# Optimization experiments

Measured on AMD Instinct MI355X. Metric: run time of the kernel, lower is better.

Reference implementation:

```python
import jax, jax.numpy as jnp
import numpy as np

B, W, NN, EPG = 8, 16, 64, 1024   # batch, window, nodes/graph, trace-edges/graph
N = B * W * NN                     # 8192 flattened nodes
E = B * W * EPG                    # 131072 node-graph edges == trace rows
E2 = 4 * E                         # 524288 edge-graph (line-graph) edges
D_NODE = 128; D_LOG = 128; D_EDGE = 128
D_IN = D_NODE + D_LOG              # 256 = GATv2 node2node in_channels
H = 4
EPS = 1e-16                        # PyG softmax epsilon


def _lin(key, fan_in, fan_out):
    return jax.random.normal(key, (fan_in, fan_out), jnp.float32) * (1.0 / np.sqrt(fan_in))


def setup_inputs() -> dict:
    key = jax.random.key(0)
    ks = jax.random.split(key, 16)
    return {
        "x_node": jax.random.normal(ks[0], (B, W, NN, D_NODE), jnp.float32),
        "x_trace": jax.random.normal(ks[1], (B, W, EPG, D_EDGE), jnp.float32),
        "x_log": jax.random.normal(ks[2], (B, W, NN, D_LOG), jnp.float32),
        "node_adj": jax.random.randint(ks[3], (2, E), 0, N, jnp.int32),
        "edge_adj": jax.random.randint(ks[4], (2, E2), 0, E, jnp.int32),
        "edge_efea": jax.random.randint(ks[5], (E2,), 0, N, jnp.int32),
        # node2node GATv2Conv: in=256, heads=4, out/head=64, edge_dim=128
        "n2n_Wl": _lin(ks[6], D_IN, D_IN), "n2n_bl": jnp.zeros((D_IN,), jnp.float32),
        "n2n_Wr": _lin(ks[7], D_IN, D_IN), "n2n_br": jnp.zeros((D_IN,), jnp.float32),
        "n2n_We": _lin(ks[8], D_EDGE, D_IN),
        "n2n_att": jax.random.normal(ks[9], (H, D_IN // H), jnp.float32) * 0.1,
        "n2n_bias": jnp.zeros((D_IN,), jnp.float32),
        # egde2node GATv2Conv: in=128, heads=4, out/head=32, edge_dim=256
        "e2n_Wl": _lin(ks[10], D_EDGE, D_EDGE), "e2n_bl": jnp.zeros((D_EDGE,), jnp.float32),
        "e2n_Wr": _lin(ks[11], D_EDGE, D_EDGE), "e2n_br": jnp.zeros((D_EDGE,), jnp.float32),
        "e2n_We": _lin(ks[12], D_IN, D_EDGE),
        "e2n_att": jax.random.normal(ks[13], (H, D_EDGE // H), jnp.float32) * 0.1,
        "e2n_bias": jnp.zeros((D_EDGE,), jnp.float32),
    }


def gatv2(x, edge_index, edge_attr, Wl, bl, Wr, br, We, att, bias, num_nodes):
    """PyG GATv2Conv (eval mode, add_self_loops=False, concat heads)."""
    heads, C = att.shape
    src, dst = edge_index[0], edge_index[1]
    xl = (x @ Wl + bl).reshape(-1, heads, C)   # source transform [N,H,C]
    xr = (x @ Wr + br).reshape(-1, heads, C)   # target transform [N,H,C]
    e = (edge_attr @ We).reshape(-1, heads, C) # edge transform   [E,H,C]
    m = jax.nn.leaky_relu(xl[src] + xr[dst] + e, 0.2)  # [E,H,C]
    alpha = jnp.einsum('ehc,hc->eh', m, att)           # [E,H]
    amax = jax.ops.segment_max(alpha, dst, num_segments=num_nodes)
    ex = jnp.exp(alpha - amax[dst])
    denom = jax.ops.segment_sum(ex, dst, num_segments=num_nodes)
    a = ex / (denom[dst] + EPS)                        # per-target softmax
    out = jax.ops.segment_sum(a[:, :, None] * xl[src], dst, num_segments=num_nodes)
    return out.reshape(num_nodes, heads * C) + bias


def reference(x_node, x_trace, x_log, node_adj, edge_adj, edge_efea,
              n2n_Wl, n2n_bl, n2n_Wr, n2n_br, n2n_We, n2n_att, n2n_bias,
              e2n_Wl, e2n_bl, e2n_Wr, e2n_br, e2n_We, e2n_att, e2n_bias):
    node = jnp.concatenate([x_node, x_log], axis=-1).reshape(-1, D_IN)  # [N,256]
    trace = x_trace.reshape(-1, D_EDGE)                                 # [E,128]
    node = gatv2(node, node_adj, trace,
                 n2n_Wl, n2n_bl, n2n_Wr, n2n_br, n2n_We, n2n_att, n2n_bias, N)
    trace = gatv2(trace, edge_adj, node[edge_efea],
                  e2n_Wl, e2n_bl, e2n_Wr, e2n_br, e2n_We, e2n_att, e2n_bias, E)
    xn = node[:, :D_NODE].reshape(B, W, NN, D_NODE)
    xt = trace.reshape(B, W, EPG, D_EDGE)
    xlg = node[:, D_NODE:].reshape(B, W, NN, D_LOG)
    return (xn, xt, xlg)
```

## Files before the change

### kernel.cpp

```cpp
#include <hip/hip_runtime.h>
#include <hip/hip_bf16.h>

constexpr int N    = 8192;
constexpr int E    = 131072;
constexpr int E2   = 524288;

constexpr size_t XT_OFF  = (size_t)N * 128;
constexpr size_t XLG_OFF = XT_OFF + (size_t)E * 128;

typedef unsigned short u16;
typedef short s16x8 __attribute__((ext_vector_type(8)));
typedef float f32x4 __attribute__((ext_vector_type(4)));

__device__ __forceinline__ u16 f2bs(float f) {
    unsigned x = __float_as_uint(f);
    return (u16)((x + 0x7FFF + ((x >> 16) & 1)) >> 16);
}
__device__ __forceinline__ float bs2f(u16 u) {
    return __uint_as_float((unsigned)u << 16);
}

__global__ __launch_bounds__(256) void k_prep(
    const float* __restrict__ Wl, const float* __restrict__ Wr,
    const float* __restrict__ We, const float* __restrict__ Wl2,
    const float* __restrict__ Wr2, const float* __restrict__ We2,
    u16* __restrict__ Wlt, u16* __restrict__ Wrt, u16* __restrict__ Wet,
    u16* __restrict__ Wl2t, u16* __restrict__ Wr2t, u16* __restrict__ We2t)
{
    const int gid = blockIdx.x * 256 + threadIdx.x;
    const float* src; u16* dst; int base, Kk, sh, perm;
    if      (gid <  65536) { src = Wl;  dst = Wlt;  base = 0;      Kk = 256; sh = 8; perm = 0; }
    else if (gid < 131072) { src = Wr;  dst = Wrt;  base = 65536;  Kk = 256; sh = 8; perm = 0; }
    else if (gid < 163840) { src = We;  dst = Wet;  base = 131072; Kk = 128; sh = 8; perm = 1; }
    else if (gid < 180224) { src = Wl2; dst = Wl2t; base = 163840; Kk = 128; sh = 7; perm = 1; }
    else if (gid < 196608) { src = Wr2; dst = Wr2t; base = 180224; Kk = 128; sh = 7; perm = 1; }
    else                   { src = We2; dst = We2t; base = 196608; Kk = 256; sh = 7; perm = 0; }
    const int l = gid - base;
    const int k = l >> sh, nn = l & ((1 << sh) - 1);
    int ns = nn;
    if (perm) ns = (nn & ~63) | ((nn & 3) << 4) | ((nn >> 2) & 15);
    dst[(size_t)ns * Kk + k] = f2bs(src[l]);
}

__global__ void k_hist2(const int* __restrict__ d1, const int* __restrict__ d2,
                        int* __restrict__ c1, int* __restrict__ c2)
{
    int i = blockIdx.x * 256 + threadIdx.x;
    if (i < E) atomicAdd(&c1[d1[i]], 1);
    else { int j = i - E; atomicAdd(&c2[d2[j]], 1); }
}

__global__ __launch_bounds__(1024) void k_scan_part(
    const int* __restrict__ cnt, int* __restrict__ off, int* __restrict__ tsums)
{
    __shared__ int tile[8192];
    __shared__ int wsum[16];
    const int tid = threadIdx.x, lane = tid & 63, wv = tid >> 6;
    const int base = blockIdx.x * 8192;
    for (int i = tid; i < 8192; i += 1024) tile[i] = cnt[base + i];
    __syncthreads();
    const int st = tid * 8;
    int s = 0;
    for (int k = 0; k < 8; ++k) { int v = tile[st + k]; tile[st + k] = s; s += v; }
    const int tsum = s;
    int incl = s;
    for (int o = 1; o < 64; o <<= 1) {
        int v = __shfl_up(incl, o);
        if (lane >= o) incl += v;
    }
    if (lane == 63) wsum[wv] = incl;
    __syncthreads();
    int woff = 0;
    for (int wq = 0; wq < wv; ++wq) woff += wsum[wq];
    const int add = woff + incl - tsum;
    for (int k = 0; k < 8; ++k) off[base + st + k] = add + tile[st + k];
    if (tid == 1023) tsums[blockIdx.x] = woff + incl;
}

__global__ __launch_bounds__(1024) void k_scan_add(
    int* __restrict__ off, int* __restrict__ cur,
    const int* __restrict__ tsums, int ntiles, int n)
{
    const int b = blockIdx.x;
    int carry = 0;
    for (int t = 0; t < b; ++t) carry += tsums[t];
    const int base = b * 8192 + threadIdx.x * 8;
#pragma unroll
    for (int k = 0; k < 8; ++k) {
        int v = off[base + k] + carry;
        off[base + k] = v;
        cur[base + k] = v;
    }
    if (b == ntiles - 1 && threadIdx.x == 1023)
        off[n] = carry + tsums[b];
}

__global__ void k_scatterM(
    const int* __restrict__ adj, int* __restrict__ cur1,
    int* __restrict__ srcc, int* __restrict__ pos1,
    const int* __restrict__ eadj, const int* __restrict__ efea,
    int* __restrict__ cur2, int2* __restrict__ sf2)
{
    int i = blockIdx.x * 256 + threadIdx.x;
    if (i < E) {
        int pos = atomicAdd(&cur1[adj[E + i]], 1);
        srcc[pos] = adj[i];
        pos1[i] = pos;
    } else {
        int j = i - E;
        int pos = atomicAdd(&cur2[eadj[E2 + j]], 1);
        sf2[pos] = make_int2(eadj[j], efea[j]);
    }
}

__global__ __launch_bounds__(256) void k_node_gemm(
    const float* __restrict__ x_node, const float* __restrict__ x_log,
    const u16* __restrict__ Wlt, const float* __restrict__ bl,
    const u16* __restrict__ Wrt, const float* __restrict__ br,
    u16* __restrict__ xl, u16* __restrict__ xr)
{
    __shared__ u16 A[32][260];
    const int n0 = blockIdx.x * 32;
    const int tid = threadIdx.x;
    for (int i = tid; i < 32 * 64; i += 256) {
        const int r = i >> 6, k4 = (i & 63) << 2;
        const float* srcp = (k4 < 128) ? &x_node[(size_t)(n0 + r) * 128 + k4]
                                       : &x_log [(size_t)(n0 + r) * 128 + (k4 - 128)];
        const float4 v = *(const float4*)srcp;
        ushort4 o; o.x = f2bs(v.x); o.y = f2bs(v.y); o.z = f2bs(v.z); o.w = f2bs(v.w);
        *(ushort4*)&A[r][k4] = o;
    }
    __syncthreads();
    const int w = tid >> 6, lane = tid & 63, lr = lane & 15, lq = lane >> 4;
    const u16* Wt     = (w < 2) ? Wlt : Wrt;
    const float* bias = (w < 2) ? bl : br;
    u16* outp         = (w < 2) ? xl : xr;
    const int cb = (w & 1) * 128;
    f32x4 acc[2][8] = {};
    for (int kb = 0; kb < 8; ++kb) {
        s16x8 afr0 = *(const s16x8*)&A[lr][kb * 32 + lq * 8];
        s16x8 afr1 = *(const s16x8*)&A[16 + lr][kb * 32 + lq * 8];
#pragma unroll
        for (int ct = 0; ct < 8; ++ct) {
            const int n = cb + ct * 16 + lr;
            s16x8 bfr = *(const s16x8*)&Wt[(size_t)n * 256 + kb * 32 + lq * 8];
            acc[0][ct] = __builtin_amdgcn_mfma_f32_16x16x32_bf16(afr0, bfr, acc[0][ct], 0, 0, 0);
            acc[1][ct] = __builtin_amdgcn_mfma_f32_16x16x32_bf16(afr1, bfr, acc[1][ct], 0, 0, 0);
        }
    }
#pragma unroll
    for (int rt = 0; rt < 2; ++rt)
#pragma unroll
        for (int ct = 0; ct < 8; ++ct) {
            const int col = cb + ct * 16 + lr;
            const float bv = bias[col];
#pragma unroll
            for (int reg = 0; reg < 4; ++reg) {
                const int row = n0 + rt * 16 + lq * 4 + reg;
                outp[(size_t)row * 256 + col] = f2bs(acc[rt][ct][reg] + bv);
            }
        }
}

constexpr int TPB_EDGE = 4;
__global__ __launch_bounds__(512) void k_edge_mm(
    const float* __restrict__ x_trace,
    const int* __restrict__ adj,
    const int* __restrict__ pos1,
    const u16* __restrict__ xl_n, const u16* __restrict__ xr_n,
    const u16* __restrict__ Wet,
    const u16* __restrict__ Wl2t, const float* __restrict__ bl2,
    const u16* __restrict__ Wr2t, const float* __restrict__ br2,
    const float* __restrict__ att,
    float* __restrict__ alpha, u16* __restrict__ xl_e, u16* __restrict__ xrst)
{
    __shared__ u16 A[2][32][132];
    __shared__ int ss[2][32], dd[2][32], pp[2][32];
    const int tid = threadIdx.x;
    const int w8 = tid >> 6;
    const int role = w8 >> 2;
    const int w = w8 & 3;
    const int lane = tid & 63, lr = lane & 15, lq = lane >> 4;

    s16x8 wf[4][4];
    const int cb2 = (w & 1) * 64;
    if (role == 0) {
#pragma unroll
        for (int kb = 0; kb < 4; ++kb)
#pragma unroll
            for (int ct = 0; ct < 4; ++ct)
                wf[kb][ct] = *(const s16x8*)&Wet[(size_t)(w * 64 + ct * 16 + lr) * 128 + kb * 32 + lq * 8];
    } else {
        const u16* Wt2 = (w < 2) ? Wl2t : Wr2t;
#pragma unroll
        for (int kb = 0; kb < 4; ++kb)
#pragma unroll
            for (int ct = 0; ct < 4; ++ct)
                wf[kb][ct] = *(const s16x8*)&Wt2[(size_t)(cb2 + ct * 16 + lr) * 128 + kb * 32 + lq * 8];
    }
    const float4 attq = *(const float4*)&att[w * 64 + lr * 4];
    const float4 b2q  = (role == 0) ? make_float4(0, 0, 0, 0)
        : *(const float4*)&((w < 2) ? bl2 : br2)[cb2 + lr * 4];

    const int tile0 = blockIdx.x * TPB_EDGE;
    {
        const int e0s = tile0 * 32;
        const int i0 = tid, i1 = tid + 512;
        {
            const int r = i0 >> 5, k4 = (i0 & 31) << 2;
            const float4 v = *(const float4*)&x_trace[(size_t)(e0s + r) * 128 + k4];
            ushort4 o; o.x = f2bs(v.x); o.y = f2bs(v.y); o.z = f2bs(v.z); o.w = f2bs(v.w);
            *(ushort4*)&A[0][r][k4] = o;
        }
        {
            const int r = i1 >> 5, k4 = (i1 & 31) << 2;
            const float4 v = *(const float4*)&x_trace[(size_t)(e0s + r) * 128 + k4];
            ushort4 o; o.x = f2bs(v.x); o.y = f2bs(v.y); o.z = f2bs(v.z); o.w = f2bs(v.w);
            *(ushort4*)&A[0][r][k4] = o;
        }
        if (tid < 32) {
            ss[0][tid] = adj[e0s + tid];
            dd[0][tid] = adj[E + e0s + tid];
            pp[0][tid] = pos1[e0s + tid];
        }
    }

    for (int t = 0; t < TPB_EDGE; ++t) {
        __syncthreads();
        const int b = t & 1;
        const int e0 = (tile0 + t) * 32;
        if (t + 1 < TPB_EDGE) {
            const int e0s = (tile0 + t + 1) * 32;
            const int bn = b ^ 1;
            {
                const int r = tid >> 5, k4 = (tid & 31) << 2;
                const float4 v = *(const float4*)&x_trace[(size_t)(e0s + r) * 128 + k4];
                ushort4 o; o.x = f2bs(v.x); o.y = f2bs(v.y); o.z = f2bs(v.z); o.w = f2bs(v.w);
                *(ushort4*)&A[bn][r][k4] = o;
            }
            {
                const int i1 = tid + 512;
                const int r = i1 >> 5, k4 = (i1 & 31) << 2;
                const float4 v = *(const float4*)&x_trace[(size_t)(e0s + r) * 128 + k4];
                ushort4 o; o.x = f2bs(v.x); o.y = f2bs(v.y); o.z = f2bs(v.z); o.w = f2bs(v.w);
                *(ushort4*)&A[bn][r][k4] = o;
            }
            if (tid < 32) {
                ss[bn][tid] = adj[e0s + tid];
                dd[bn][tid] = adj[E + e0s + tid];
                pp[bn][tid] = pos1[e0s + tid];
            }
        }

        if (role == 0) {
            const int co = w * 64 + lr * 4;
            ushort4 xlv[2][4], xrv[2][4];
#pragma unroll
            for (int rt = 0; rt < 2; ++rt)
#pragma unroll
                for (int reg = 0; reg < 4; ++reg) {
                    const int rowt = rt * 16 + lq * 4 + reg;
                    xlv[rt][reg] = *(const ushort4*)&xl_n[(size_t)ss[b][rowt] * 256 + co];
                    xrv[rt][reg] = *(const ushort4*)&xr_n[(size_t)dd[b][rowt] * 256 + co];
                }
            f32x4 acc1[2][4] = {};
#pragma unroll
            for (int kb = 0; kb < 4; ++kb) {
                s16x8 afr0 = *(const s16x8*)&A[b][lr][kb * 32 + lq * 8];
                s16x8 afr1 = *(const s16x8*)&A[b][16 + lr][kb * 32 + lq * 8];
#pragma unroll
                for (int ct = 0; ct < 4; ++ct) {
                    acc1[0][ct] = __builtin_amdgcn_mfma_f32_16x16x32_bf16(afr0, wf[kb][ct], acc1[0][ct], 0, 0, 0);
                    acc1[1][ct] = __builtin_amdgcn_mfma_f32_16x16x32_bf16(afr1, wf[kb][ct], acc1[1][ct], 0, 0, 0);
                }
            }
            float sums[2][4];
#pragma unroll
            for (int rt = 0; rt < 2; ++rt)
#pragma unroll
                for (int reg = 0; reg < 4; ++reg) {
                    float m0 = acc1[rt][0][reg] + bs2f(xlv[rt][reg].x) + bs2f(xrv[rt][reg].x);
                    float m1 = acc1[rt][1][reg] + bs2f(xlv[rt][reg].y) + bs2f(xrv[rt][reg].y);
                    float m2 = acc1[rt][2][reg] + bs2f(xlv[rt][reg].z) + bs2f(xrv[rt][reg].z);
                    float m3 = acc1[rt][3][reg] + bs2f(xlv[rt][reg].w) + bs2f(xrv[rt][reg].w);
                    m0 = m0 > 0.f ? m0 : 0.2f * m0;
                    m1 = m1 > 0.f ? m1 : 0.2f * m1;
                    m2 = m2 > 0.f ? m2 : 0.2f * m2;
                    m3 = m3 > 0.f ? m3 : 0.2f * m3;
                    sums[rt][reg] = m0 * attq.x + m1 * attq.y + m2 * attq.z + m3 * attq.w;
                }
#pragma unroll
            for (int rt = 0; rt < 2; ++rt)
#pragma unroll
                for (int reg = 0; reg < 4; ++reg) {
                    float p = sums[rt][reg];
                    p += __shfl_xor(p, 8);
                    p += __shfl_xor(p, 4);
                    p += __shfl_xor(p, 2);
                    p += __shfl_xor(p, 1);
                    if (lr == 0)
                        alpha[(size_t)pp[b][rt * 16 + lq * 4 + reg] * 4 + w] = p;
                }
        } else {
            f32x4 acc2[2][4] = {};
#pragma unroll
            for (int kb = 0; kb < 4; ++kb) {
                s16x8 afr0 = *(const s16x8*)&A[b][lr][kb * 32 + lq * 8];
                s16x8 afr1 = *(const s16x8*)&A[b][16 + lr][kb * 32 + lq * 8];
#pragma unroll
                for (int ct = 0; ct < 4; ++ct) {
                    acc2[0][ct] = __builtin_amdgcn_mfma_f32_16x16x32_bf16(afr0, wf[kb][ct], acc2[0][ct], 0, 0, 0);
                    acc2[1][ct] = __builtin_amdgcn_mfma_f32_16x16x32_bf16(afr1, wf[kb][ct], acc2[1][ct], 0, 0, 0);
                }
            }
#pragma unroll
            for (int rt = 0; rt < 2; ++rt)
#pragma unroll
                for (int reg = 0; reg < 4; ++reg) {
                    const int row = e0 + rt * 16 + lq * 4 + reg;
                    ushort4 o;
                    o.x = f2bs(acc2[rt][0][reg] + b2q.x);
                    o.y = f2bs(acc2[rt][1][reg] + b2q.y);
                    o.z = f2bs(acc2[rt][2][reg] + b2q.z);
                    o.w = f2bs(acc2[rt][3][reg] + b2q.w);
                    if (w < 2) *(ushort4*)&xl_e[(size_t)row * 128 + cb2 + lr * 4] = o;
                    else       *(ushort4*)&xrst[(size_t)row * 256 + cb2 + lr * 4] = o;
                }
        }
    }
}

__global__ __launch_bounds__(256) void k_fused1(
    const int* __restrict__ off, const int* __restrict__ srcc,
    const float* __restrict__ alphac,
    const u16* __restrict__ xl,
    const float* __restrict__ bias,
    float* __restrict__ out)
{
    const int wv = __builtin_amdgcn_readfirstlane(threadIdx.x >> 6);
    const int lane = threadIdx.x & 63;
    const int n = blockIdx.x * 4 + wv;
    const int c = lane * 4;
    const int h = lane >> 4;
    const int beg = off[n], end = off[n + 1];
    float mx = -INFINITY, den = 0.f;
    float a0 = 0.f, a1 = 0.f, a2 = 0.f, a3 = 0.f;
    int i = beg;
    while (i < end) {
        const int rem = end - i;
        int sa[8]; float pe[8];
#pragma unroll
        for (int k = 0; k < 8; ++k) {
            const int idx = i + (k < rem ? k : rem - 1);
            sa[k] = srcc[idx];
            pe[k] = alphac[(size_t)idx * 4 + h];
        }
        ushort4 xv[8];
#pragma unroll
        for (int k = 0; k < 8; ++k)
            xv[k] = *(const ushort4*)&xl[(size_t)sa[k] * 256 + c];
#pragma unroll
        for (int k = 0; k < 8; ++k) {
            const float p = (k < rem) ? pe[k] : -INFINITY;
            const float mnew = fmaxf(mx, p);
            const float sc = __expf(mx - mnew);
            const float ex = __expf(p - mnew);
            den = den * sc + ex;
            a0 = a0 * sc + ex * bs2f(xv[k].x);
            a1 = a1 * sc + ex * bs2f(xv[k].y);
            a2 = a2 * sc + ex * bs2f(xv[k].z);
            a3 = a3 * sc + ex * bs2f(xv[k].w);
            mx = mnew;
        }
        i += 8;
    }
    const float inv = 1.f / (den + 1e-16f);
    float4 r;
    r.x = a0 * inv + bias[c + 0];
    r.y = a1 * inv + bias[c + 1];
    r.z = a2 * inv + bias[c + 2];
    r.w = a3 * inv + bias[c + 3];
    if (lane < 32) *(float4*)&out[(size_t)n * 128 + c] = r;
    else           *(float4*)&out[XLG_OFF + (size_t)n * 128 + (c - 128)] = r;
}

__global__ __launch_bounds__(256) void k_proj_gemm(
    const float* __restrict__ out_node, const u16* __restrict__ We2t,
    u16* __restrict__ proj)
{
    __shared__ u16 A[32][260];
    const int n0 = blockIdx.x * 32;
    const int tid = threadIdx.x;
    for (int i = tid; i < 32 * 64; i += 256) {
        const int r = i >> 6, k4 = (i & 63) << 2;
        const float* srcp = (k4 < 128)
            ? &out_node[(size_t)(n0 + r) * 128 + k4]
            : &out_node[XLG_OFF + (size_t)(n0 + r) * 128 + (k4 - 128)];
        const float4 v = *(const float4*)srcp;
        ushort4 o; o.x = f2bs(v.x); o.y = f2bs(v.y); o.z = f2bs(v.z); o.w = f2bs(v.w);
        *(ushort4*)&A[r][k4] = o;
    }
    __syncthreads();
    const int w = tid >> 6, lane = tid & 63, lr = lane & 15, lq = lane >> 4;
    f32x4 acc[2][2] = {};
    for (int kb = 0; kb < 8; ++kb) {
        s16x8 afr0 = *(const s16x8*)&A[lr][kb * 32 + lq * 8];
        s16x8 afr1 = *(const s16x8*)&A[16 + lr][kb * 32 + lq * 8];
#pragma unroll
        for (int ct = 0; ct < 2; ++ct) {
            const int col = w * 32 + ct * 16 + lr;
            s16x8 bfr = *(const s16x8*)&We2t[(size_t)col * 256 + kb * 32 + lq * 8];
            acc[0][ct] = __builtin_amdgcn_mfma_f32_16x16x32_bf16(afr0, bfr, acc[0][ct], 0, 0, 0);
            acc[1][ct] = __builtin_amdgcn_mfma_f32_16x16x32_bf16(afr1, bfr, acc[1][ct], 0, 0, 0);
        }
    }
#pragma unroll
    for (int rt = 0; rt < 2; ++rt)
#pragma unroll
        for (int ct = 0; ct < 2; ++ct) {
            const int col = w * 32 + ct * 16 + lr;
#pragma unroll
            for (int reg = 0; reg < 4; ++reg) {
                const int row = n0 + rt * 16 + lq * 4 + reg;
                proj[(size_t)row * 128 + col] = f2bs(acc[rt][ct][reg]);
            }
        }
}

__global__ __launch_bounds__(256) void k_fused2(
    const int* __restrict__ off, const int2* __restrict__ sf2,
    const u16* __restrict__ xl,
    const u16* __restrict__ proj,
    const float* __restrict__ att,
    const float* __restrict__ bias,
    float* __restrict__ out)
{
    const int wv = __builtin_amdgcn_readfirstlane(threadIdx.x >> 6);
    const int lane = threadIdx.x & 63;
    const int d = blockIdx.x * 4 + wv;
    const int c = lane * 2;
    const u16* xrst = (const u16*)(out + XT_OFF);
    const unsigned xrp = *(const unsigned*)&xrst[(size_t)d * 256 + c];
    const float xr0 = bs2f((u16)(xrp & 0xffff));
    const float xr1 = bs2f((u16)(xrp >> 16));
    const float av0 = att[c], av1 = att[c + 1];
    const int beg = off[d], end = off[d + 1];
    float mx = -INFINITY, den = 0.f, a0 = 0.f, a1 = 0.f;
    int i = beg;
    while (i < end) {
        const int rem = end - i;
        int2 sf[4];
#pragma unroll
        for (int k = 0; k < 4; ++k) sf[k] = sf2[i + (k < rem ? k : rem - 1)];
        unsigned xv[4], pv[4];
#pragma unroll
        for (int k = 0; k < 4; ++k) {
            xv[k] = *(const unsigned*)&xl[(size_t)sf[k].x * 128 + c];
            pv[k] = *(const unsigned*)&proj[(size_t)sf[k].y * 128 + c];
        }
#pragma unroll
        for (int k = 0; k < 4; ++k) {
            const float x0 = bs2f((u16)(xv[k] & 0xffff));
            const float x1 = bs2f((u16)(xv[k] >> 16));
            float m0 = x0 + xr0 + bs2f((u16)(pv[k] & 0xffff));
            float m1 = x1 + xr1 + bs2f((u16)(pv[k] >> 16));
            m0 = m0 > 0.f ? m0 : 0.2f * m0;
            m1 = m1 > 0.f ? m1 : 0.2f * m1;
            float pp = m0 * av0 + m1 * av1;
            pp += __shfl_xor(pp, 8, 16);
            pp += __shfl_xor(pp, 4, 16);
            pp += __shfl_xor(pp, 2, 16);
            pp += __shfl_xor(pp, 1, 16);
            const float p = (k < rem) ? pp : -INFINITY;
            const float mnew = fmaxf(mx, p);
            const float sc = __expf(mx - mnew);
            const float ex = __expf(p - mnew);
            den = den * sc + ex;
            a0 = a0 * sc + ex * x0;
            a1 = a1 * sc + ex * x1;
            mx = mnew;
        }
        i += 4;
    }
    const float inv = 1.f / (den + 1e-16f);
    float2 o2;
    o2.x = a0 * inv + bias[c];
    o2.y = a1 * inv + bias[c + 1];
    *(float2*)&out[XT_OFF + (size_t)d * 128 + c] = o2;
}

extern "C" void kernel_launch(void* const* d_in, const int* in_sizes, int n_in,
                              void* d_out, int out_size, void* d_ws, size_t ws_size,
                              hipStream_t stream)
{
    const float* x_node   = (const float*)d_in[0];
    const float* x_trace  = (const float*)d_in[1];
    const float* x_log    = (const float*)d_in[2];
    const int*   node_adj = (const int*)d_in[3];
    const int*   edge_adj = (const int*)d_in[4];
    const int*   efea     = (const int*)d_in[5];
    const float* n2n_Wl   = (const float*)d_in[6];
    const float* n2n_bl   = (const float*)d_in[7];
    const float* n2n_Wr   = (const float*)d_in[8];
    const float* n2n_br   = (const float*)d_in[9];
    const float* n2n_We   = (const float*)d_in[10];
    const float* n2n_att  = (const float*)d_in[11];
    const float* n2n_bias = (const float*)d_in[12];
    const float* e2n_Wl   = (const float*)d_in[13];
    const float* e2n_bl   = (const float*)d_in[14];
    const float* e2n_Wr   = (const float*)d_in[15];
    const float* e2n_br   = (const float*)d_in[16];
    const float* e2n_We   = (const float*)d_in[17];
    const float* e2n_att  = (const float*)d_in[18];
    const float* e2n_bias = (const float*)d_in[19];
    float* out = (float*)d_out;

    char* w = (char*)d_ws;
    int*  cnt1   = (int*)w;   w += (size_t)N * 4;
    int*  cnt2   = (int*)w;   w += (size_t)E * 4;
    int*  off1   = (int*)w;   w += (size_t)(N + 4) * 4;
    int*  cur1   = (int*)w;   w += (size_t)N * 4;
    int*  src1   = (int*)w;   w += (size_t)E * 4;
    int*  pos1   = (int*)w;   w += (size_t)E * 4;
    float* alphac = (float*)w; w += (size_t)E * 4 * 4;
    int*  off2   = (int*)w;   w += (size_t)(E + 4) * 4;
    int*  cur2   = (int*)w;   w += (size_t)E * 4;
    int2* sf2    = (int2*)w;  w += (size_t)E2 * 8;
    u16*  xl_n   = (u16*)w;   w += (size_t)N * 256 * 2;
    u16*  xr_n   = (u16*)w;   w += (size_t)N * 256 * 2;
    u16*  xl_e   = (u16*)w;   w += (size_t)E * 128 * 2;
    u16*  proj   = (u16*)w;   w += (size_t)N * 128 * 2;
    u16*  Wlt    = (u16*)w;   w += (size_t)65536 * 2;
    u16*  Wrt    = (u16*)w;   w += (size_t)65536 * 2;
    u16*  Wet    = (u16*)w;   w += (size_t)32768 * 2;
    u16*  Wl2t   = (u16*)w;   w += (size_t)16384 * 2;
    u16*  Wr2t   = (u16*)w;   w += (size_t)16384 * 2;
    u16*  We2t   = (u16*)w;   w += (size_t)32768 * 2;
    int*  tsum1  = (int*)w;   w += 64;
    int*  tsum2  = (int*)w;   w += 64;

    hipMemsetAsync(d_ws, 0, (size_t)(N + E) * 4, stream);

    k_prep<<<896, 256, 0, stream>>>(n2n_Wl, n2n_Wr, n2n_We, e2n_Wl, e2n_Wr, e2n_We,
                                    Wlt, Wrt, Wet, Wl2t, Wr2t, We2t);
    k_hist2<<<(E + E2) / 256, 256, 0, stream>>>(node_adj + E, edge_adj + E2, cnt1, cnt2);
    k_scan_part<<<N / 8192, 1024, 0, stream>>>(cnt1, off1, tsum1);
    k_scan_part<<<E / 8192, 1024, 0, stream>>>(cnt2, off2, tsum2);
    k_scan_add<<<N / 8192, 1024, 0, stream>>>(off1, cur1, tsum1, N / 8192, N);
    k_scan_add<<<E / 8192, 1024, 0, stream>>>(off2, cur2, tsum2, E / 8192, E);
    k_scatterM<<<(E + E2) / 256, 256, 0, stream>>>(node_adj, cur1, src1, pos1,
                                                   edge_adj, efea, cur2, sf2);

    k_node_gemm<<<N / 32, 256, 0, stream>>>(x_node, x_log, Wlt, n2n_bl, Wrt, n2n_br,
                                            xl_n, xr_n);
    k_edge_mm<<<E / (32 * TPB_EDGE), 512, 0, stream>>>(x_trace, node_adj, pos1, xl_n, xr_n,
                                          Wet, Wl2t, e2n_bl, Wr2t, e2n_br,
                                          n2n_att, alphac, xl_e, (u16*)(out + XT_OFF));
    k_fused1<<<N / 4, 256, 0, stream>>>(off1, src1, alphac, xl_n, n2n_bias, out);

    k_proj_gemm<<<N / 32, 256, 0, stream>>>(out, We2t, proj);
    k_fused2<<<E / 4, 256, 0, stream>>>(off2, sf2, xl_e, proj,
                                        e2n_att, e2n_bias, out);
}
```

Measured before the change: 400.4 us.

## Merge setup kernels and fuse projection GEMM into node aggregation kernel

Merges weight prep and histogram into one setup kernel, and merges the two scans and two scan-adds into combined launches that handle both graphs. Fuses the node-output projection GEMM into the node aggregation kernel. The fused kernel uses 1024-thread blocks of 16 nodes, stages the bf16 results in LDS, and runs an MFMA on 8 of its 16 waves. This cuts launch count and avoids re-reading the fp32 node output, but leaves half the waves idle during the GEMM and lowers per-block parallelism.

Result: faster. 387.6 us (-3.2%).

```diff
diff --git a/kernel.cpp b/kernel.cpp
--- a/kernel.cpp
+++ b/kernel.cpp
@@ -20,43 +20,47 @@
     return __uint_as_float((unsigned)u << 16);
 }
 
-__global__ __launch_bounds__(256) void k_prep(
+__global__ __launch_bounds__(256) void k_setup(
     const float* __restrict__ Wl, const float* __restrict__ Wr,
     const float* __restrict__ We, const float* __restrict__ Wl2,
     const float* __restrict__ Wr2, const float* __restrict__ We2,
     u16* __restrict__ Wlt, u16* __restrict__ Wrt, u16* __restrict__ Wet,
-    u16* __restrict__ Wl2t, u16* __restrict__ Wr2t, u16* __restrict__ We2t)
+    u16* __restrict__ Wl2t, u16* __restrict__ Wr2t, u16* __restrict__ We2t,
+    const int* __restrict__ d1, const int* __restrict__ d2,
+    int* __restrict__ c1, int* __restrict__ c2)
 {
     const int gid = blockIdx.x * 256 + threadIdx.x;
-    const float* src; u16* dst; int base, Kk, sh, perm;
-    if      (gid <  65536) { src = Wl;  dst = Wlt;  base = 0;      Kk = 256; sh = 8; perm = 0; }
-    else if (gid < 131072) { src = Wr;  dst = Wrt;  base = 65536;  Kk = 256; sh = 8; perm = 0; }
-    else if (gid < 163840) { src = We;  dst = Wet;  base = 131072; Kk = 128; sh = 8; perm = 1; }
-    else if (gid < 180224) { src = Wl2; dst = Wl2t; base = 163840; Kk = 128; sh = 7; perm = 1; }
-    else if (gid < 196608) { src = Wr2; dst = Wr2t; base = 180224; Kk = 128; sh = 7; perm = 1; }
-    else                   { src = We2; dst = We2t; base = 196608; Kk = 256; sh = 7; perm = 0; }
-    const int l = gid - base;
-    const int k = l >> sh, nn = l & ((1 << sh) - 1);
-    int ns = nn;
-    if (perm) ns = (nn & ~63) | ((nn & 3) << 4) | ((nn >> 2) & 15);
-    dst[(size_t)ns * Kk + k] = f2bs(src[l]);
-}
-
-__global__ void k_hist2(const int* __restrict__ d1, const int* __restrict__ d2,
-                        int* __restrict__ c1, int* __restrict__ c2)
-{
-    int i = blockIdx.x * 256 + threadIdx.x;
-    if (i < E) atomicAdd(&c1[d1[i]], 1);
-    else { int j = i - E; atomicAdd(&c2[d2[j]], 1); }
-}
-
-__global__ __launch_bounds__(1024) void k_scan_part(
-    const int* __restrict__ cnt, int* __restrict__ off, int* __restrict__ tsums)
+    if (gid < 229376) {
+        const float* src; u16* dst; int base, Kk, sh, perm;
+        if      (gid <  65536) { src = Wl;  dst = Wlt;  base = 0;      Kk = 256; sh = 8; perm = 0; }
+        else if (gid < 131072) { src = Wr;  dst = Wrt;  base = 65536;  Kk = 256; sh = 8; perm = 0; }
+        else if (gid < 163840) { src = We;  dst = Wet;  base = 131072; Kk = 128; sh = 8; perm = 1; }
+        else if (gid < 180224) { src = Wl2; dst = Wl2t; base = 163840; Kk = 128; sh = 7; perm = 1; }
+        else if (gid < 196608) { src = Wr2; dst = Wr2t; base = 180224; Kk = 128; sh = 7; perm = 1; }
+        else                   { src = We2; dst = We2t; base = 196608; Kk = 256; sh = 7; perm = 0; }
+        const int l = gid - base;
+        const int k = l >> sh, nn = l & ((1 << sh) - 1);
+        int ns = nn;
+        if (perm) ns = (nn & ~63) | ((nn & 3) << 4) | ((nn >> 2) & 15);
+        dst[(size_t)ns * Kk + k] = f2bs(src[l]);
+    } else {
+        const int j = gid - 229376;
+        if (j < E) atomicAdd(&c1[d1[j]], 1);
+        else       atomicAdd(&c2[d2[j - E]], 1);
+    }
+}
+
+__global__ __launch_bounds__(1024) void k_scan_part2(
+    const int* __restrict__ cnt1, int* __restrict__ off1, int* __restrict__ tsum1,
+    const int* __restrict__ cnt2, int* __restrict__ off2, int* __restrict__ tsum2)
 {
     __shared__ int tile[8192];
     __shared__ int wsum[16];
     const int tid = threadIdx.x, lane = tid & 63, wv = tid >> 6;
-    const int base = blockIdx.x * 8192;
+    const int b = blockIdx.x;
+    const int* cnt; int* off; int* tsums; int base, tb;
+    if (b == 0) { cnt = cnt1; off = off1; tsums = tsum1; base = 0; tb = 0; }
+    else        { cnt = cnt2; off = off2; tsums = tsum2; base = (b - 1) * 8192; tb = b - 1; }
     for (int i = tid; i < 8192; i += 1024) tile[i] = cnt[base + i];
     __syncthreads();
     const int st = tid * 8;
@@ -74,25 +78,33 @@
     for (int wq = 0; wq < wv; ++wq) woff += wsum[wq];
     const int add = woff + incl - tsum;
     for (int k = 0; k < 8; ++k) off[base + st + k] = add + tile[st + k];
-    if (tid == 1023) tsums[blockIdx.x] = woff + incl;
-}
-
-__global__ __launch_bounds__(1024) void k_scan_add(
-    int* __restrict__ off, int* __restrict__ cur,
-    const int* __restrict__ tsums, int ntiles, int n)
+    if (tid == 1023) tsums[tb] = woff + incl;
+}
+
+__global__ __launch_bounds__(1024) void k_scan_add2(
+    int* __restrict__ off1, int* __restrict__ cur1, const int* __restrict__ tsum1,
+    int* __restrict__ off2, int* __restrict__ cur2, const int* __restrict__ tsum2)
 {
     const int b = blockIdx.x;
-    int carry = 0;
-    for (int t = 0; t < b; ++t) carry += tsums[t];
-    const int base = b * 8192 + threadIdx.x * 8;
-#pragma unroll
-    for (int k = 0; k < 8; ++k) {
-        int v = off[base + k] + carry;
-        off[base + k] = v;
-        cur[base + k] = v;
-    }
-    if (b == ntiles - 1 && threadIdx.x == 1023)
-        off[n] = carry + tsums[b];
+    if (b == 0) {
+        const int base = threadIdx.x * 8;
+#pragma unroll
+        for (int k = 0; k < 8; ++k) cur1[base + k] = off1[base + k];
+        if (threadIdx.x == 1023) off1[N] = tsum1[0];
+    } else {
+        const int tb = b - 1;
+        int carry = 0;
+        for (int t = 0; t < tb; ++t) carry += tsum2[t];
+        const int base = tb * 8192 + threadIdx.x * 8;
+#pragma unroll
+        for (int k = 0; k < 8; ++k) {
+            int v = off2[base + k] + carry;
+            off2[base + k] = v;
+            cur2[base + k] = v;
+        }
+        if (tb == E / 8192 - 1 && threadIdx.x == 1023)
+            off2[E] = carry + tsum2[tb];
+    }
 }
 
 __global__ void k_scatterM(
@@ -330,16 +342,19 @@
     }
 }
 
-__global__ __launch_bounds__(256) void k_fused1(
+__global__ __launch_bounds__(1024) void k_fused1(
     const int* __restrict__ off, const int* __restrict__ srcc,
     const float* __restrict__ alphac,
     const u16* __restrict__ xl,
     const float* __restrict__ bias,
-    float* __restrict__ out)
-{
+    const u16* __restrict__ We2t,
+    float* __restrict__ out, u16* __restrict__ proj)
+{
+    __shared__ u16 Alds[16][264];
     const int wv = __builtin_amdgcn_readfirstlane(threadIdx.x >> 6);
     const int lane = threadIdx.x & 63;
-    const int n = blockIdx.x * 4 + wv;
+    const int n0 = blockIdx.x * 16;
+    const int n = n0 + wv;
     const int c = lane * 4;
     const int h = lane >> 4;
     const int beg = off[n], end = off[n + 1];
@@ -382,49 +397,26 @@
     r.w = a3 * inv + bias[c + 3];
     if (lane < 32) *(float4*)&out[(size_t)n * 128 + c] = r;
     else           *(float4*)&out[XLG_OFF + (size_t)n * 128 + (c - 128)] = r;
-}
-
-__global__ __launch_bounds__(256) void k_proj_gemm(
-    const float* __restrict__ out_node, const u16* __restrict__ We2t,
-    u16* __restrict__ proj)
-{
-    __shared__ u16 A[32][260];
-    const int n0 = blockIdx.x * 32;
-    const int tid = threadIdx.x;
-    for (int i = tid; i < 32 * 64; i += 256) {
-        const int r = i >> 6, k4 = (i & 63) << 2;
-        const float* srcp = (k4 < 128)
-            ? &out_node[(size_t)(n0 + r) * 128 + k4]
-            : &out_node[XLG_OFF + (size_t)(n0 + r) * 128 + (k4 - 128)];
-        const float4 v = *(const float4*)srcp;
-        ushort4 o; o.x = f2bs(v.x); o.y = f2bs(v.y); o.z = f2bs(v.z); o.w = f2bs(v.w);
-        *(ushort4*)&A[r][k4] = o;
+    {
+        ushort4 o; o.x = f2bs(r.x); o.y = f2bs(r.y); o.z = f2bs(r.z); o.w = f2bs(r.w);
+        *(ushort4*)&Alds[wv][c] = o;
     }
     __syncthreads();
-    const int w = tid >> 6, lane = tid & 63, lr = lane & 15, lq = lane >> 4;
-    f32x4 acc[2][2] = {};
-    for (int kb = 0; kb < 8; ++kb) {
-        s16x8 afr0 = *(const s16x8*)&A[lr][kb * 32 + lq * 8];
-        s16x8 afr1 = *(const s16x8*)&A[16 + lr][kb * 32 + lq * 8];
-#pragma unroll
-        for (int ct = 0; ct < 2; ++ct) {
-            const int col = w * 32 + ct * 16 + lr;
-            s16x8 bfr = *(const s16x8*)&We2t[(size_t)col * 256 + kb * 32 + lq * 8];
-            acc[0][ct] = __builtin_amdgcn_mfma_f32_16x16x32_bf16(afr0, bfr, acc[0][ct], 0, 0, 0);
-            acc[1][ct] = __builtin_amdgcn_mfma_f32_16x16x32_bf16(afr1, bfr, acc[1][ct], 0, 0, 0);
-        }
-    }
-#pragma unroll
-    for (int rt = 0; rt < 2; ++rt)
-#pragma unroll
-        for (int ct = 0; ct < 2; ++ct) {
-            const int col = w * 32 + ct * 16 + lr;
-#pragma unroll
-            for (int reg = 0; reg < 4; ++reg) {
-                const int row = n0 + rt * 16 + lq * 4 + reg;
-                proj[(size_t)row * 128 + col] = f2bs(acc[rt][ct][reg]);
-            }
-        }
+    if (wv < 8) {
+        const int lr = lane & 15, lq = lane >> 4;
+        const int colb = wv * 16;
+        f32x4 acc = {};
+        for (int kb = 0; kb < 8; ++kb) {
+            s16x8 afr = *(const s16x8*)&Alds[lr][kb * 32 + lq * 8];
+            s16x8 bfr = *(const s16x8*)&We2t[(size_t)(colb + lr) * 256 + kb * 32 + lq * 8];
+            acc = __builtin_amdgcn_mfma_f32_16x16x32_bf16(afr, bfr, acc, 0, 0, 0);
+        }
+#pragma unroll
+        for (int reg = 0; reg < 4; ++reg) {
+            const int row = n0 + lq * 4 + reg;
+            proj[(size_t)row * 128 + colb + lr] = f2bs(acc[reg]);
+        }
+    }
 }
 
 __global__ __launch_bounds__(256) void k_fused2(
@@ -541,13 +533,11 @@
 
     hipMemsetAsync(d_ws, 0, (size_t)(N + E) * 4, stream);
 
-    k_prep<<<896, 256, 0, stream>>>(n2n_Wl, n2n_Wr, n2n_We, e2n_Wl, e2n_Wr, e2n_We,
-                                    Wlt, Wrt, Wet, Wl2t, Wr2t, We2t);
-    k_hist2<<<(E + E2) / 256, 256, 0, stream>>>(node_adj + E, edge_adj + E2, cnt1, cnt2);
-    k_scan_part<<<N / 8192, 1024, 0, stream>>>(cnt1, off1, tsum1);
-    k_scan_part<<<E / 8192, 1024, 0, stream>>>(cnt2, off2, tsum2);
-    k_scan_add<<<N / 8192, 1024, 0, stream>>>(off1, cur1, tsum1, N / 8192, N);
-    k_scan_add<<<E / 8192, 1024, 0, stream>>>(off2, cur2, tsum2, E / 8192, E);
+    k_setup<<<3456, 256, 0, stream>>>(n2n_Wl, n2n_Wr, n2n_We, e2n_Wl, e2n_Wr, e2n_We,
+                                      Wlt, Wrt, Wet, Wl2t, Wr2t, We2t,
+                                      node_adj + E, edge_adj + E2, cnt1, cnt2);
+    k_scan_part2<<<1 + E / 8192, 1024, 0, stream>>>(cnt1, off1, tsum1, cnt2, off2, tsum2);
+    k_scan_add2<<<1 + E / 8192, 1024, 0, stream>>>(off1, cur1, tsum1, off2, cur2, tsum2);
     k_scatterM<<<(E + E2) / 256, 256, 0, stream>>>(node_adj, cur1, src1, pos1,
                                                    edge_adj, efea, cur2, sf2);
 
@@ -556,9 +546,9 @@
     k_edge_mm<<<E / (32 * TPB_EDGE), 512, 0, stream>>>(x_trace, node_adj, pos1, xl_n, xr_n,
                                           Wet, Wl2t, e2n_bl, Wr2t, e2n_br,
                                           n2n_att, alphac, xl_e, (u16*)(out + XT_OFF));
-    k_fused1<<<N / 4, 256, 0, stream>>>(off1, src1, alphac, xl_n, n2n_bias, out);
-
-    k_proj_gemm<<<N / 32, 256, 0, stream>>>(out, We2t, proj);
+    k_fused1<<<N / 16, 1024, 0, stream>>>(off1, src1, alphac, xl_n, n2n_bias,
+                                          We2t, out, proj);
+
     k_fused2<<<E / 4, 256, 0, stream>>>(off2, sf2, xl_e, proj,
                                         e2n_att, e2n_bias, out);
 }
```
